# Performance work log

Hardware: AMD Instinct MI355X
Metric: run time of the kernel (lower is better)

The kernel has to match this reference:

```python
import jax, jax.numpy as jnp
import numpy as np
from jax import lax

B, W, M = 4, 20, 512
RNN_HID = 64
N_HIDDEN = RNN_HID          # bi = False
HALF = N_HIDDEN // 2
K = 10
LONG_K = W // 2             # conv_long kernel
LONG_OUT = W - 2 * (LONG_K - 1)   # = 2
N_SPATIAL = 10


def setup_inputs() -> dict:
    key = jax.random.key(0)
    ks = jax.random.split(key, 24)
    g = lambda i, shape, s=0.05: jax.random.normal(ks[i], shape, jnp.float32) * s
    return {
        "x": jax.random.normal(ks[0], (B, W, M), jnp.float32),
        # vanilla RNN (tanh), 1 layer, input_size=1
        "W_ih": g(1, (RNN_HID, 1), 0.2), "W_hh": g(2, (RNN_HID, RNN_HID), 0.1),
        "b_ih": g(3, (RNN_HID,)), "b_hh": g(4, (RNN_HID,)),
        # attention adjacency params
        "W1": g(5, (HALF, N_HIDDEN), 0.1), "b1": g(6, (HALF,)),
        "W2": g(7, (HALF, N_HIDDEN), 0.1),
        "V": g(8, (HALF,), 0.1), "bv": g(9, (1,)),
        "Wb": g(10, (M, M), 0.05), "wb": g(11, (1,)),
        # conv / conv_long
        "conv_w": g(12, (K, 1, W), 0.1), "conv_b": g(13, (K,)),
        "convl_w": g(14, (K, 1, LONG_K), 0.1), "convl_b": g(15, (K,)),
        # graph conv layers: adj @ (x @ W) + b
        "gc1_w": g(16, ((1 + LONG_OUT) * K, N_HIDDEN), 0.1), "gc1_b": g(17, (N_HIDDEN,)),
        "gc2_w": g(18, (N_HIDDEN, N_SPATIAL), 0.1), "gc2_b": g(19, (N_SPATIAL,)),
        # output head
        "out_w": g(20, (1, N_HIDDEN + N_SPATIAL), 0.1), "out_b": g(21, (1,)),
        # fixed geographic adjacency (data.adj)
        "adj": jax.random.uniform(ks[22], (M, M), dtype=jnp.float32),
    }


def _conv1d(x, w, b, dilation=1):
    # x: (N, Cin, W), w: (Cout, Cin, K) -> (N, Cout, Wout), VALID padding
    y = lax.conv_general_dilated(x, w, (1,), 'VALID', rhs_dilation=(dilation,),
                                 dimension_numbers=('NCH', 'OIH', 'NCH'))
    return y + b[None, :, None]


def reference(x, W_ih, W_hh, b_ih, b_hh, W1, b1, W2, V, bv, Wb, wb,
              conv_w, conv_b, convl_w, convl_b, gc1_w, gc1_b, gc2_w, gc2_b,
              out_w, out_b, adj):
    b, w, m = x.shape
    # ---- RNN encode each node's scalar series: (b*m, w, 1) -> last hidden ----
    xr = jnp.transpose(x, (0, 2, 1)).reshape(b * m, w)          # (bm, w)
    inp = xr[..., None] @ W_ih.T + b_ih                         # (bm, w, H)

    def step(h, u):
        return jnp.tanh(u + h @ W_hh.T + b_hh), None

    h0 = jnp.zeros((b * m, RNN_HID), x.dtype)
    h_last, _ = lax.scan(step, h0, jnp.swapaxes(inp, 0, 1))     # (bm, H)
    last_hid = h_last.reshape(b, m, N_HIDDEN)
    out_temporal = last_hid

    # ---- pairwise bilinear attention adjacency (broadcast instead of repeat) ----
    p = last_hid @ W1.T                                         # (b, m, H/2)
    q = last_hid @ W2.T                                         # (b, m, H/2)
    e = jax.nn.elu(p[:, :, None, :] + q[:, None, :, :] + b1)    # (b, m, m, H/2)
    a_mx = e @ V + bv[0]                                        # (b, m, m)
    # F.normalize(p=2, dim=1)
    nrm = jnp.maximum(jnp.sqrt(jnp.sum(a_mx * a_mx, axis=1, keepdims=True)), 1e-12)
    a_mx = a_mx / nrm
    c = jax.nn.sigmoid(a_mx @ Wb + wb[0])                       # (b, m, m)
    A = adj[None] * c + a_mx * (1.0 - c)

    # ---- per-node convs, batched over all b*m series (no Python loop) ----
    h_tmp = xr[:, None, :]                                      # (bm, 1, w)
    r = _conv1d(h_tmp, conv_w, conv_b)                          # (bm, k, 1)
    r_long = _conv1d(h_tmp, convl_w, convl_b, dilation=2)       # (bm, k, long_out)
    r_l = jnp.concatenate([r, r_long], axis=-1).reshape(b, m, -1)  # (b, m, (1+lo)*k)
    r_l = jax.nn.relu(r_l)

    # ---- graph convolutions: adj @ (x @ W) + b ----
    xg = jax.nn.relu(A @ (r_l @ gc1_w) + gc1_b)                 # (b, m, H)
    out_spatial = jax.nn.relu(A @ (xg @ gc2_w) + gc2_b)         # (b, m, 10)

    out = jnp.concatenate([out_spatial, out_temporal], axis=-1)
    return (out @ out_w.T + out_b)[..., 0]                      # (b, m)
```

## Files before the change

kernel.cpp:

```cpp
#include <hip/hip_runtime.h>
#include <hip/hip_bf16.h>
#include <cstdint>
#include <cstddef>

#define OFF_P     0
#define OFF_QB    65536
#define OFF_TDOT  131072
#define OFF_COLSQ 133120
#define OFF_ZT    135168
#define OFF_G1B   155648
#define OFF_AMXB  221184
#define OFF_WBT   745472
#define OFF_ABF   1269760
#define OFF_G1T   1794048

typedef __attribute__((ext_vector_type(8))) short short8;
typedef __attribute__((ext_vector_type(8))) unsigned short ushort8;
typedef __attribute__((ext_vector_type(4))) float f32x4;

__device__ inline unsigned short f2bf(float f) {
    unsigned u = __builtin_bit_cast(unsigned, f);
    unsigned r = u + 0x7FFFu + ((u >> 16) & 1u);
    return (unsigned short)(r >> 16);
}
__device__ inline float bf2f(unsigned short s) {
    unsigned u = ((unsigned)s) << 16;
    return __builtin_bit_cast(float, u);
}
__device__ inline float tanh_fast(float x) {
    return 1.f - 2.f/(__expf(2.f*x) + 1.f);
}

__global__ __launch_bounds__(256) void k1_rnn(
    const float* __restrict__ x, const float* __restrict__ W_ih,
    const float* __restrict__ W_hh, const float* __restrict__ b_ih,
    const float* __restrict__ b_hh, const float* __restrict__ W1,
    const float* __restrict__ b1, const float* __restrict__ W2,
    const float* __restrict__ conv_w, const float* __restrict__ conv_b,
    const float* __restrict__ convl_w, const float* __restrict__ convl_b,
    const float* __restrict__ gc1_w, const float* __restrict__ out_w,
    const float* __restrict__ out_b,
    float* __restrict__ p_out, float* __restrict__ qb_out,
    unsigned short* __restrict__ G1bf, float* __restrict__ tdot,
    float* __restrict__ colsq)
{
    __shared__ float h_sh[4][64];
    __shared__ float xt_sh[4][20];
    __shared__ float rl_sh[4][30];
    int tid = threadIdx.x;
    int w = tid >> 6, lane = tid & 63;
    int s = blockIdx.x * 4 + w;
    int b = s >> 9, m = s & 511;

    if (blockIdx.x < 8) colsq[blockIdx.x * 256 + tid] = 0.f;

    if (lane < 20) xt_sh[w][lane] = x[(b*20 + lane)*512 + m];

    float wrow[64];
    const float* wr = W_hh + lane*64;
    #pragma unroll
    for (int k4 = 0; k4 < 16; ++k4) {
        float4 v = reinterpret_cast<const float4*>(wr)[k4];
        wrow[4*k4+0]=v.x; wrow[4*k4+1]=v.y; wrow[4*k4+2]=v.z; wrow[4*k4+3]=v.w;
    }
    float wih = W_ih[lane], bih = b_ih[lane], bhh = b_hh[lane];
    h_sh[w][lane] = 0.f;
    float h = 0.f;

    if (lane < 10) {
        float acc = conv_b[lane];
        #pragma unroll
        for (int t = 0; t < 20; ++t) acc += conv_w[lane*20+t]*xt_sh[w][t];
        rl_sh[w][3*lane] = fmaxf(acc, 0.f);
    } else if (lane < 30) {
        int idx = lane-10, j = idx>>1, oo = idx&1;
        float acc = convl_b[j];
        #pragma unroll
        for (int t = 0; t < 10; ++t) acc += convl_w[j*10+t]*xt_sh[w][oo+2*t];
        rl_sh[w][3*j+1+oo] = fmaxf(acc, 0.f);
    }

    for (int t = 0; t < 20; ++t) {
        float acc = xt_sh[w][t]*wih + bih + bhh;
        #pragma unroll
        for (int k = 0; k < 64; ++k) acc += wrow[k]*h_sh[w][k];
        h = tanh_fast(acc);
        h_sh[w][lane] = h;
    }

    float td = h * out_w[10 + lane];
    #pragma unroll
    for (int off = 32; off; off >>= 1) td += __shfl_down(td, off);
    if (lane == 0) tdot[s] = td + out_b[0];

    if (lane < 32) {
        const float* w1r = W1 + lane*64;
        float acc = 0.f;
        #pragma unroll
        for (int k = 0; k < 64; ++k) acc += w1r[k]*h_sh[w][k];
        p_out[s*32 + lane] = acc;
    } else {
        int i = lane - 32;
        const float* w2r = W2 + i*64;
        float acc = 0.f;
        #pragma unroll
        for (int k = 0; k < 64; ++k) acc += w2r[k]*h_sh[w][k];
        qb_out[s*32 + i] = acc + b1[i];
    }

    float g = 0.f;
    #pragma unroll
    for (int t = 0; t < 30; ++t) g += rl_sh[w][t]*gc1_w[t*64 + lane];
    G1bf[s*64 + lane] = f2bf(g);
}

__global__ __launch_bounds__(256) void k2_amx(
    const float* __restrict__ p, const float* __restrict__ qb,
    const float* __restrict__ V, const float* __restrict__ bv,
    unsigned short* __restrict__ amxB, float* __restrict__ colsq)
{
    __shared__ float p_sh[32*36], q_sh[32*36], v_sh[32], sq_sh[32*17];
    int t = threadIdx.x;
    int b = blockIdx.z, i0 = blockIdx.y*32, j0 = blockIdx.x*32;
    {
        int r = t >> 3, c4 = (t & 7)*4;
        *(float4*)&p_sh[r*36 + c4] = *(const float4*)(p  + (size_t)(b*512 + i0 + r)*32 + c4);
        *(float4*)&q_sh[r*36 + c4] = *(const float4*)(qb + (size_t)(b*512 + j0 + r)*32 + c4);
    }
    if (t < 32) v_sh[t] = V[t];
    __syncthreads();

    int ti = t >> 4, tj = t & 15;
    float bv0 = bv[0];
    float a00 = bv0, a01 = bv0, a10 = bv0, a11 = bv0;
    #pragma unroll
    for (int h = 0; h < 32; ++h) {
        float p0 = p_sh[ti*36 + h], p1 = p_sh[(ti+16)*36 + h];
        float q0 = q_sh[tj*36 + h], q1 = q_sh[(tj+16)*36 + h];
        float vh = v_sh[h];
        float x00 = p0+q0, x01 = p0+q1, x10 = p1+q0, x11 = p1+q1;
        float e00 = x00 > 0.f ? x00 : __expf(x00)-1.f;
        float e01 = x01 > 0.f ? x01 : __expf(x01)-1.f;
        float e10 = x10 > 0.f ? x10 : __expf(x10)-1.f;
        float e11 = x11 > 0.f ? x11 : __expf(x11)-1.f;
        a00 += vh*e00; a01 += vh*e01; a10 += vh*e10; a11 += vh*e11;
    }
    size_t base0 = ((size_t)(b*512 + i0 + ti))*512 + j0;
    size_t base1 = ((size_t)(b*512 + i0 + ti + 16))*512 + j0;
    amxB[base0 + tj]      = f2bf(a00);
    amxB[base0 + tj + 16] = f2bf(a01);
    amxB[base1 + tj]      = f2bf(a10);
    amxB[base1 + tj + 16] = f2bf(a11);

    sq_sh[tj*17 + ti]      = a00*a00 + a10*a10;
    sq_sh[(tj+16)*17 + ti] = a01*a01 + a11*a11;
    __syncthreads();
    if (t < 32) {
        float ssum = 0.f;
        #pragma unroll
        for (int r = 0; r < 16; ++r) ssum += sq_sh[t*17 + r];
        atomicAdd(&colsq[b*512 + j0 + t], ssum);
    }
}

__global__ __launch_bounds__(256) void k2w_scale(
    const float* __restrict__ Wb, const float* __restrict__ colsq,
    const unsigned short* __restrict__ G1bf,
    unsigned short* __restrict__ WbT, unsigned short* __restrict__ G1T)
{
    __shared__ float tile[64][68];
    __shared__ unsigned short ttile[64*72];
    int t = threadIdx.x;

    if (blockIdx.y == 8) {
        int bb = blockIdx.x;
        int b = bb >> 1;
        int j0base = (bb & 1) * 256;
        for (int chunk = 0; chunk < 4; ++chunk) {
            int j0 = j0base + chunk*64;
            {
                int jr = t >> 2, c0 = (t & 3)*16;
                const unsigned short* src = G1bf + ((size_t)(b*512 + j0 + jr))*64 + c0;
                *(short8*)&ttile[jr*72 + c0]     = *(const short8*)src;
                *(short8*)&ttile[jr*72 + c0 + 8] = *(const short8*)(src + 8);
            }
            __syncthreads();
            {
                int c = t >> 2, jc = (t & 3)*16;
                ushort8 v0, v1;
                #pragma unroll
                for (int q = 0; q < 8; ++q) v0[q] = ttile[(jc+q)*72 + c];
                #pragma unroll
                for (int q = 0; q < 8; ++q) v1[q] = ttile[(jc+8+q)*72 + c];
                unsigned short* dst = G1T + ((size_t)(b*64 + c))*512 + j0 + jc;
                *(ushort8*)dst = v0;
                *(ushort8*)(dst+8) = v1;
            }
            __syncthreads();
        }
        return;
    }

    int j0 = blockIdx.x*64, k0 = blockIdx.y*64;
    #pragma unroll
    for (int q = 0; q < 4; ++q) {
        int kr = (t>>4) + 16*q;
        int jc = (t&15)*4;
        *(float4*)&tile[kr][jc] = *(const float4*)(Wb + (size_t)(k0+kr)*512 + j0 + jc);
    }
    __syncthreads();
    int jl = t>>2, kc = (t&3)*16;
    int j = j0 + jl;
    for (int b = 0; b < 4; ++b) {
        ushort8 v0, v1;
        #pragma unroll
        for (int kk = 0; kk < 8; ++kk) {
            float inv = 1.f/fmaxf(sqrtf(colsq[b*512 + k0+kc+kk]), 1e-12f);
            v0[kk] = f2bf(tile[kc+kk][jl] * inv);
        }
        #pragma unroll
        for (int kk = 0; kk < 8; ++kk) {
            float inv = 1.f/fmaxf(sqrtf(colsq[b*512 + k0+kc+8+kk]), 1e-12f);
            v1[kk] = f2bf(tile[kc+8+kk][jl] * inv);
        }
        unsigned short* dst = WbT + ((size_t)(b*512 + j))*512 + k0 + kc;
        *(ushort8*)dst = v0;
        *(ushort8*)(dst+8) = v1;
    }
}

__global__ __launch_bounds__(64) void k3a_mfma(
    const unsigned short* __restrict__ amxB, const unsigned short* __restrict__ WbT,
    const float* __restrict__ colsq, const float* __restrict__ wb,
    const float* __restrict__ adj, unsigned short* __restrict__ Abf)
{
    int lane = threadIdx.x;
    int b = blockIdx.z;
    int i0 = blockIdx.y*32, j0 = blockIdx.x*32;
    f32x4 acc[2][2] = {};

    const unsigned short* abase = amxB + ((size_t)(b*512 + i0 + (lane&15)))*512 + (lane>>4)*8;
    const unsigned short* bbase = WbT  + ((size_t)(b*512 + j0 + (lane&15)))*512 + (lane>>4)*8;

    #pragma unroll 4
    for (int k0 = 0; k0 < 512; k0 += 32) {
        short8 a0 = *(const short8*)(abase + k0);
        short8 a1 = *(const short8*)(abase + 16*512 + k0);
        short8 b0 = *(const short8*)(bbase + k0);
        short8 b1 = *(const short8*)(bbase + 16*512 + k0);
        acc[0][0] = __builtin_amdgcn_mfma_f32_16x16x32_bf16(a0, b0, acc[0][0],0,0,0);
        acc[0][1] = __builtin_amdgcn_mfma_f32_16x16x32_bf16(a0, b1, acc[0][1],0,0,0);
        acc[1][0] = __builtin_amdgcn_mfma_f32_16x16x32_bf16(a1, b0, acc[1][0],0,0,0);
        acc[1][1] = __builtin_amdgcn_mfma_f32_16x16x32_bf16(a1, b1, acc[1][1],0,0,0);
    }

    float wbs = wb[0];
    #pragma unroll
    for (int fj = 0; fj < 2; ++fj) {
        int j = j0 + fj*16 + (lane&15);
        float inv = 1.f/fmaxf(sqrtf(colsq[b*512 + j]), 1e-12f);
        #pragma unroll
        for (int fi = 0; fi < 2; ++fi)
        #pragma unroll
        for (int r = 0; r < 4; ++r) {
            int i = i0 + fi*16 + (lane>>4)*4 + r;
            float S = acc[fi][fj][r] + wbs;
            float c = 1.f/(1.f + __expf(-S));
            float aN = bf2f(amxB[((size_t)(b*512)+i)*512 + j]) * inv;
            Abf[((size_t)(b*512)+i)*512 + j] = f2bf(adj[i*512+j]*c + aN*(1.f - c));
        }
    }
}

#define AS_STRIDE 520
__global__ __launch_bounds__(256) void k3b_mfma(
    const unsigned short* __restrict__ Abf, const unsigned short* __restrict__ G1T,
    const float* __restrict__ gc1_b, const float* __restrict__ gc2_w,
    float* __restrict__ zT)
{
    __shared__ __align__(16) unsigned short As[16*AS_STRIDE];
    __shared__ float xg[16][68];
    int t = threadIdx.x;
    int b = blockIdx.y, i0 = blockIdx.x*16;
    int wv = t >> 6, lane = t & 63;

    {
        int r = t >> 4, seg = (t & 15)*32;
        const unsigned short* src = Abf + ((size_t)(b*512 + i0 + r))*512 + seg;
        *(short8*)&As[r*AS_STRIDE + seg]      = *(const short8*)src;
        *(short8*)&As[r*AS_STRIDE + seg + 8]  = *(const short8*)(src + 8);
        *(short8*)&As[r*AS_STRIDE + seg + 16] = *(const short8*)(src + 16);
        *(short8*)&As[r*AS_STRIDE + seg + 24] = *(const short8*)(src + 24);
    }
    __syncthreads();

    f32x4 acc = {};
    const unsigned short* gbase = G1T + ((size_t)(b*64 + wv*16 + (lane&15)))*512 + (lane>>4)*8;
    int aoff = (lane&15)*AS_STRIDE + (lane>>4)*8;
    #pragma unroll 4
    for (int k0 = 0; k0 < 512; k0 += 32) {
        short8 af = *(const short8*)&As[aoff + k0];
        short8 bf = *(const short8*)(gbase + k0);
        acc = __builtin_amdgcn_mfma_f32_16x16x32_bf16(af, bf, acc, 0,0,0);
    }

    {
        int cc = wv*16 + (lane&15);
        float gb = gc1_b[cc];
        #pragma unroll
        for (int r = 0; r < 4; ++r)
            xg[(lane>>4)*4 + r][cc] = fmaxf(acc[r] + gb, 0.f);
    }
    __syncthreads();

    if (t < 160) {
        int row = t/10, sx = t%10;
        float a = 0.f;
        #pragma unroll
        for (int c = 0; c < 64; ++c) a += xg[row][c]*gc2_w[c*10 + sx];
        zT[((size_t)(b*10) + sx)*512 + i0 + row] = a;
    }
}

__global__ __launch_bounds__(256) void k4_out(
    const unsigned short* __restrict__ Abf, const float* __restrict__ zT,
    const float* __restrict__ gc2_b, const float* __restrict__ out_w,
    const float* __restrict__ tdot, float* __restrict__ out)
{
    int t = threadIdx.x;
    int w = t >> 6, lane = t & 63;
    int s = blockIdx.x*4 + w;
    int b = s >> 9;

    short8 av = *(const short8*)(Abf + (size_t)s*512 + lane*8);
    float a[8];
    #pragma unroll
    for (int q = 0; q < 8; ++q) a[q] = bf2f((unsigned short)av[q]);

    float acc[10];
    #pragma unroll
    for (int sx = 0; sx < 10; ++sx) {
        const float* zr = zT + ((size_t)(b*10) + sx)*512 + lane*8;
        float4 z0 = *(const float4*)zr;
        float4 z1 = *(const float4*)(zr + 4);
        acc[sx] = a[0]*z0.x + a[1]*z0.y + a[2]*z0.z + a[3]*z0.w
                + a[4]*z1.x + a[5]*z1.y + a[6]*z1.z + a[7]*z1.w;
    }
    #pragma unroll
    for (int sx = 0; sx < 10; ++sx)
        #pragma unroll
        for (int off = 32; off; off >>= 1) acc[sx] += __shfl_down(acc[sx], off);
    if (lane == 0) {
        float o = tdot[s];
        #pragma unroll
        for (int sx = 0; sx < 10; ++sx)
            o += fmaxf(acc[sx] + gc2_b[sx], 0.f) * out_w[sx];
        out[s] = o;
    }
}

extern "C" void kernel_launch(void* const* d_in, const int* in_sizes, int n_in,
                              void* d_out, int out_size, void* d_ws, size_t ws_size,
                              hipStream_t stream) {
    const float* x       = (const float*)d_in[0];
    const float* W_ih    = (const float*)d_in[1];
    const float* W_hh    = (const float*)d_in[2];
    const float* b_ih    = (const float*)d_in[3];
    const float* b_hh    = (const float*)d_in[4];
    const float* W1      = (const float*)d_in[5];
    const float* b1      = (const float*)d_in[6];
    const float* W2      = (const float*)d_in[7];
    const float* V       = (const float*)d_in[8];
    const float* bv      = (const float*)d_in[9];
    const float* Wb      = (const float*)d_in[10];
    const float* wb      = (const float*)d_in[11];
    const float* conv_w  = (const float*)d_in[12];
    const float* conv_b  = (const float*)d_in[13];
    const float* convl_w = (const float*)d_in[14];
    const float* convl_b = (const float*)d_in[15];
    const float* gc1_w   = (const float*)d_in[16];
    const float* gc1_b   = (const float*)d_in[17];
    const float* gc2_w   = (const float*)d_in[18];
    const float* gc2_b   = (const float*)d_in[19];
    const float* out_w   = (const float*)d_in[20];
    const float* out_b   = (const float*)d_in[21];
    const float* adj     = (const float*)d_in[22];

    float* ws    = (float*)d_ws;
    float* p     = ws + OFF_P;
    float* qb    = ws + OFF_QB;
    float* tdot  = ws + OFF_TDOT;
    float* colsq = ws + OFF_COLSQ;
    float* zT    = ws + OFF_ZT;
    unsigned short* G1bf = (unsigned short*)(ws + OFF_G1B);
    unsigned short* amxB = (unsigned short*)(ws + OFF_AMXB);
    unsigned short* WbT  = (unsigned short*)(ws + OFF_WBT);
    unsigned short* Abf  = (unsigned short*)(ws + OFF_ABF);
    unsigned short* G1T  = (unsigned short*)(ws + OFF_G1T);
    float* out   = (float*)d_out;

    k1_rnn<<<dim3(512), dim3(256), 0, stream>>>(
        x, W_ih, W_hh, b_ih, b_hh, W1, b1, W2,
        conv_w, conv_b, convl_w, convl_b, gc1_w, out_w, out_b,
        p, qb, G1bf, tdot, colsq);

    k2_amx<<<dim3(16,16,4), dim3(256), 0, stream>>>(p, qb, V, bv, amxB, colsq);
    k2w_scale<<<dim3(8,9), dim3(256), 0, stream>>>(Wb, colsq, G1bf, WbT, G1T);

    k3a_mfma<<<dim3(16,16,4), dim3(64), 0, stream>>>(amxB, WbT, colsq, wb, adj, Abf);
    k3b_mfma<<<dim3(32,4), dim3(256), 0, stream>>>(Abf, G1T, gc1_b, gc2_w, zT);
    k4_out<<<dim3(512), dim3(256), 0, stream>>>(Abf, zT, gc2_b, out_w, tdot, out);
}
```

Measured before the change: 70.89 us.

## Fuse Wb normalization into attention GEMM and write G1 transposed directly

Removes the k2w_scale kernel. The per-batch normalized, transposed bf16 copy of Wb is now built on the fly inside k3a_mfma: it reads fp32 Wb columns, scales them by rsqrt of the column norms and converts to bf16 per k-step. The RNN kernel now writes G1 straight into the transposed layout instead of going through a separate transpose pass. This saves one launch and a large intermediate buffer, but k3a now does strided fp32 global loads and redundant conversion work in every block.

```diff
diff --git a/kernel.cpp b/kernel.cpp
--- a/kernel.cpp
+++ b/kernel.cpp
@@ -8,11 +8,9 @@
 #define OFF_TDOT  131072
 #define OFF_COLSQ 133120
 #define OFF_ZT    135168
-#define OFF_G1B   155648
-#define OFF_AMXB  221184
-#define OFF_WBT   745472
-#define OFF_ABF   1269760
-#define OFF_G1T   1794048
+#define OFF_AMXB  155648
+#define OFF_ABF   679936
+#define OFF_G1T   1204224
 
 typedef __attribute__((ext_vector_type(8))) short short8;
 typedef __attribute__((ext_vector_type(8))) unsigned short ushort8;
@@ -41,7 +39,7 @@
     const float* __restrict__ gc1_w, const float* __restrict__ out_w,
     const float* __restrict__ out_b,
     float* __restrict__ p_out, float* __restrict__ qb_out,
-    unsigned short* __restrict__ G1bf, float* __restrict__ tdot,
+    unsigned short* __restrict__ G1T, float* __restrict__ tdot,
     float* __restrict__ colsq)
 {
     __shared__ float h_sh[4][64];
@@ -111,7 +109,7 @@
     float g = 0.f;
     #pragma unroll
     for (int t = 0; t < 30; ++t) g += rl_sh[w][t]*gc1_w[t*64 + lane];
-    G1bf[s*64 + lane] = f2bf(g);
+    G1T[((size_t)(b*64 + lane))*512 + m] = f2bf(g);
 }
 
 __global__ __launch_bounds__(256) void k2_amx(
@@ -163,74 +161,8 @@
     }
 }
 
-__global__ __launch_bounds__(256) void k2w_scale(
-    const float* __restrict__ Wb, const float* __restrict__ colsq,
-    const unsigned short* __restrict__ G1bf,
-    unsigned short* __restrict__ WbT, unsigned short* __restrict__ G1T)
-{
-    __shared__ float tile[64][68];
-    __shared__ unsigned short ttile[64*72];
-    int t = threadIdx.x;
-
-    if (blockIdx.y == 8) {
-        int bb = blockIdx.x;
-        int b = bb >> 1;
-        int j0base = (bb & 1) * 256;
-        for (int chunk = 0; chunk < 4; ++chunk) {
-            int j0 = j0base + chunk*64;
-            {
-                int jr = t >> 2, c0 = (t & 3)*16;
-                const unsigned short* src = G1bf + ((size_t)(b*512 + j0 + jr))*64 + c0;
-                *(short8*)&ttile[jr*72 + c0]     = *(const short8*)src;
-                *(short8*)&ttile[jr*72 + c0 + 8] = *(const short8*)(src + 8);
-            }
-            __syncthreads();
-            {
-                int c = t >> 2, jc = (t & 3)*16;
-                ushort8 v0, v1;
-                #pragma unroll
-                for (int q = 0; q < 8; ++q) v0[q] = ttile[(jc+q)*72 + c];
-                #pragma unroll
-                for (int q = 0; q < 8; ++q) v1[q] = ttile[(jc+8+q)*72 + c];
-                unsigned short* dst = G1T + ((size_t)(b*64 + c))*512 + j0 + jc;
-                *(ushort8*)dst = v0;
-                *(ushort8*)(dst+8) = v1;
-            }
-            __syncthreads();
-        }
-        return;
-    }
-
-    int j0 = blockIdx.x*64, k0 = blockIdx.y*64;
-    #pragma unroll
-    for (int q = 0; q < 4; ++q) {
-        int kr = (t>>4) + 16*q;
-        int jc = (t&15)*4;
-        *(float4*)&tile[kr][jc] = *(const float4*)(Wb + (size_t)(k0+kr)*512 + j0 + jc);
-    }
-    __syncthreads();
-    int jl = t>>2, kc = (t&3)*16;
-    int j = j0 + jl;
-    for (int b = 0; b < 4; ++b) {
-        ushort8 v0, v1;
-        #pragma unroll
-        for (int kk = 0; kk < 8; ++kk) {
-            float inv = 1.f/fmaxf(sqrtf(colsq[b*512 + k0+kc+kk]), 1e-12f);
-            v0[kk] = f2bf(tile[kc+kk][jl] * inv);
-        }
-        #pragma unroll
-        for (int kk = 0; kk < 8; ++kk) {
-            float inv = 1.f/fmaxf(sqrtf(colsq[b*512 + k0+kc+8+kk]), 1e-12f);
-            v1[kk] = f2bf(tile[kc+8+kk][jl] * inv);
-        }
-        unsigned short* dst = WbT + ((size_t)(b*512 + j))*512 + k0 + kc;
-        *(ushort8*)dst = v0;
-        *(ushort8*)(dst+8) = v1;
-    }
-}
-
 __global__ __launch_bounds__(64) void k3a_mfma(
-    const unsigned short* __restrict__ amxB, const unsigned short* __restrict__ WbT,
+    const unsigned short* __restrict__ amxB, const float* __restrict__ Wb,
     const float* __restrict__ colsq, const float* __restrict__ wb,
     const float* __restrict__ adj, unsigned short* __restrict__ Abf)
 {
@@ -239,15 +171,32 @@
     int i0 = blockIdx.y*32, j0 = blockIdx.x*32;
     f32x4 acc[2][2] = {};
 
-    const unsigned short* abase = amxB + ((size_t)(b*512 + i0 + (lane&15)))*512 + (lane>>4)*8;
-    const unsigned short* bbase = WbT  + ((size_t)(b*512 + j0 + (lane&15)))*512 + (lane>>4)*8;
-
-    #pragma unroll 4
+    int kslice = (lane>>4)*8;
+    int fr = lane & 15;
+    const unsigned short* abase = amxB + ((size_t)(b*512 + i0 + fr))*512 + kslice;
+    const float* wcol = Wb + j0 + fr;
+    const float* csq  = colsq + b*512 + kslice;
+
     for (int k0 = 0; k0 < 512; k0 += 32) {
+        float4 c0 = *(const float4*)(csq + k0);
+        float4 c1 = *(const float4*)(csq + k0 + 4);
+        float inv[8] = {
+            rsqrtf(fmaxf(c0.x,1e-24f)), rsqrtf(fmaxf(c0.y,1e-24f)),
+            rsqrtf(fmaxf(c0.z,1e-24f)), rsqrtf(fmaxf(c0.w,1e-24f)),
+            rsqrtf(fmaxf(c1.x,1e-24f)), rsqrtf(fmaxf(c1.y,1e-24f)),
+            rsqrtf(fmaxf(c1.z,1e-24f)), rsqrtf(fmaxf(c1.w,1e-24f)) };
+
         short8 a0 = *(const short8*)(abase + k0);
         short8 a1 = *(const short8*)(abase + 16*512 + k0);
-        short8 b0 = *(const short8*)(bbase + k0);
-        short8 b1 = *(const short8*)(bbase + 16*512 + k0);
+
+        const float* wk = wcol + (size_t)(k0 + kslice)*512;
+        short8 b0, b1;
+        #pragma unroll
+        for (int m = 0; m < 8; ++m) {
+            b0[m] = (short)f2bf(wk[(size_t)m*512]      * inv[m]);
+            b1[m] = (short)f2bf(wk[(size_t)m*512 + 16] * inv[m]);
+        }
+
         acc[0][0] = __builtin_amdgcn_mfma_f32_16x16x32_bf16(a0, b0, acc[0][0],0,0,0);
         acc[0][1] = __builtin_amdgcn_mfma_f32_16x16x32_bf16(a0, b1, acc[0][1],0,0,0);
         acc[1][0] = __builtin_amdgcn_mfma_f32_16x16x32_bf16(a1, b0, acc[1][0],0,0,0);
@@ -257,8 +206,8 @@
     float wbs = wb[0];
     #pragma unroll
     for (int fj = 0; fj < 2; ++fj) {
-        int j = j0 + fj*16 + (lane&15);
-        float inv = 1.f/fmaxf(sqrtf(colsq[b*512 + j]), 1e-12f);
+        int j = j0 + fj*16 + fr;
+        float inv = rsqrtf(fmaxf(colsq[b*512 + j], 1e-24f));
         #pragma unroll
         for (int fi = 0; fi < 2; ++fi)
         #pragma unroll
@@ -392,9 +341,7 @@
     float* tdot  = ws + OFF_TDOT;
     float* colsq = ws + OFF_COLSQ;
     float* zT    = ws + OFF_ZT;
-    unsigned short* G1bf = (unsigned short*)(ws + OFF_G1B);
     unsigned short* amxB = (unsigned short*)(ws + OFF_AMXB);
-    unsigned short* WbT  = (unsigned short*)(ws + OFF_WBT);
     unsigned short* Abf  = (unsigned short*)(ws + OFF_ABF);
     unsigned short* G1T  = (unsigned short*)(ws + OFF_G1T);
     float* out   = (float*)d_out;
@@ -402,12 +349,11 @@
     k1_rnn<<<dim3(512), dim3(256), 0, stream>>>(
         x, W_ih, W_hh, b_ih, b_hh, W1, b1, W2,
         conv_w, conv_b, convl_w, convl_b, gc1_w, out_w, out_b,
-        p, qb, G1bf, tdot, colsq);
+        p, qb, G1T, tdot, colsq);
 
     k2_amx<<<dim3(16,16,4), dim3(256), 0, stream>>>(p, qb, V, bv, amxB, colsq);
-    k2w_scale<<<dim3(8,9), dim3(256), 0, stream>>>(Wb, colsq, G1bf, WbT, G1T);
-
-    k3a_mfma<<<dim3(16,16,4), dim3(64), 0, stream>>>(amxB, WbT, colsq, wb, adj, Abf);
+
+    k3a_mfma<<<dim3(16,16,4), dim3(64), 0, stream>>>(amxB, Wb, colsq, wb, adj, Abf);
     k3b_mfma<<<dim3(32,4), dim3(256), 0, stream>>>(Abf, G1T, gc1_b, gc2_w, zT);
     k4_out<<<dim3(512), dim3(256), 0, stream>>>(Abf, zT, gc2_b, out_w, tdot, out);
 }
```

New measurement: 59.42 us, median of 2. 1.19x faster.
